# Optimization experiments

Hardware: AMD Instinct MI355X
Metric: run time of the kernel (lower is better)

Reference implementation:

```python
import jax, jax.numpy as jnp
import numpy as np

C, H, O, T, B = 15, 256, 512, 60, 1024


def setup_inputs() -> dict:
    key = jax.random.key(0)
    ks = jax.random.split(key, 8)
    s = 1.0 / np.sqrt(H)
    return {
        "x": jax.random.normal(ks[0], (B, H), dtype=jnp.float32),
        "cam": jax.random.randint(ks[1], (B,), 0, C, dtype=jnp.int32),
        "W_ih": jax.random.uniform(ks[2], (C, 3 * H, H), jnp.float32, -s, s),
        "W_hh": jax.random.uniform(ks[3], (C, 3 * H, H), jnp.float32, -s, s),
        "b_ih": jax.random.uniform(ks[4], (C, 3 * H), jnp.float32, -s, s),
        "b_hh": jax.random.uniform(ks[5], (C, 3 * H), jnp.float32, -s, s),
        "Wc": jax.random.uniform(ks[6], (C, O, H), jnp.float32, -s, s),
        "bc": jax.random.uniform(ks[7], (C, O), jnp.float32, -s, s),
    }


def reference(x, cam, W_ih, W_hh, b_ih, b_hh, Wc, bc):
    # Gather per-sample (per-camera) parameters once.
    Wi = W_ih[cam]          # [B, 3H, H]
    Wh = W_hh[cam]          # [B, 3H, H]
    bi = b_ih[cam]          # [B, 3H]
    bh = b_hh[cam]          # [B, 3H]
    Wcs = Wc[cam]           # [B, O, H]
    bcs = bc[cam]           # [B, O]

    # Input is constant across timesteps -> input gate preactivations computed once.
    gi = jnp.einsum('bh,bgh->bg', x, Wi) + bi   # [B, 3H]
    gi_r, gi_z, gi_n = jnp.split(gi, 3, axis=1)

    h0 = jnp.zeros_like(x)  # [B, H]

    def step(h, _):
        gh = jnp.einsum('bh,bgh->bg', h, Wh) + bh
        gh_r, gh_z, gh_n = jnp.split(gh, 3, axis=1)
        r = jax.nn.sigmoid(gi_r + gh_r)
        z = jax.nn.sigmoid(gi_z + gh_z)
        n = jnp.tanh(gi_n + r * gh_n)
        h_new = (1.0 - z) * n + z * h
        out = jax.nn.sigmoid(jnp.einsum('bh,boh->bo', h_new, Wcs) + bcs)  # [B, O]
        return h_new, out

    _, outs = jax.lax.scan(step, h0, None, length=T)  # [T, B, O]
    return jnp.transpose(outs, (1, 2, 0))             # [B, O, T]
```

## Files before the change

### kernel.cpp

```cpp
#include <hip/hip_runtime.h>
#include <hip/hip_fp16.h>

#define C_    15
#define H_    256
#define O_    512
#define T_    60
#define B_    1024
#define G3H_  768
#define TS    16
#define MAXG  12
#define NSLOT 96
#define NU    80
#define PACKB 300
#define CVTB  2880

typedef __attribute__((ext_vector_type(8))) short bf16x8;
typedef __attribute__((ext_vector_type(4))) float f32x4;

__device__ __forceinline__ unsigned short f2bf(float f) {
    union { float f; unsigned u; } v; v.f = f;
    return (unsigned short)((v.u + 0x7FFFu + ((v.u >> 16) & 1u)) >> 16);
}
__device__ __forceinline__ float sigf(float x) { return 1.f / (1.f + __expf(-x)); }

__global__ __launch_bounds__(256) void prep_kernel(
    const int* __restrict__ cam, const float* __restrict__ Wih,
    const float* __restrict__ Whh, const float* __restrict__ Wc,
    int* __restrict__ order, int* __restrict__ tcam, int* __restrict__ toff,
    int* __restrict__ tcnt, unsigned short* __restrict__ Wih_b,
    unsigned short* __restrict__ Wpack)
{
    int bid = blockIdx.x, tid = threadIdx.x;
    if (bid == 0) {
        __shared__ int cnt[C_], start[C_], fill[C_];
        if (tid < C_) cnt[tid] = 0;
        if (tid < NSLOT) { tcam[tid] = -1; toff[tid] = 0; tcnt[tid] = 0; }
        __syncthreads();
        for (int b = tid; b < B_; b += 256) atomicAdd(&cnt[cam[b]], 1);
        __syncthreads();
        if (tid == 0) {
            int run = 0;
            for (int c = 0; c < C_; ++c) { start[c] = run; fill[c] = run; run += cnt[c]; }
        }
        __syncthreads();
        for (int b = tid; b < B_; b += 256) {
            int pos = atomicAdd(&fill[cam[b]], 1);
            order[pos] = b;
        }
        __syncthreads();
        if (tid == 0) {
            int gcnt[8] = {0,0,0,0,0,0,0,0};
            for (int c = 0; c < C_; ++c) gcnt[c & 7] += (cnt[c] + TS - 1) / TS;
            int maxg = 0;
            for (int g = 0; g < 8; ++g) maxg = max(maxg, gcnt[g]);
            if (maxg <= MAXG) {
                for (int g = 0; g < 8; ++g) {
                    int k = 0;
                    for (int c = g; c < C_; c += 8)
                        for (int r = 0; r < cnt[c]; r += TS) {
                            int slot = g + 8 * k;
                            tcam[slot] = c; toff[slot] = start[c] + r;
                            tcnt[slot] = min(TS, cnt[c] - r); ++k;
                        }
                }
            } else {
                int ti = 0;
                for (int c = 0; c < C_; ++c)
                    for (int r = 0; r < cnt[c]; r += TS) {
                        tcam[ti] = c; toff[ti] = start[c] + r;
                        tcnt[ti] = min(TS, cnt[c] - r); ++ti;
                    }
            }
        }
    } else if (bid <= PACKB) {
        int cu = (bid - 1) * 4 + (tid >> 6);
        int c = cu / NU, u = cu - c * NU;
        int lane = tid & 63, q = lane >> 4, l16 = lane & 15;
        const float* src = (u < 48)
            ? &Whh[((size_t)c * G3H_ + u * 16 + l16) * H_]
            : &Wc[((size_t)c * O_ + (u - 48) * 16 + l16) * H_];
        unsigned short* dst = Wpack + ((size_t)cu * 8) * 512 + lane * 8;
#pragma unroll
        for (int kk = 0; kk < 8; ++kk) {
            float4 v0 = *(const float4*)&src[kk * 32 + q * 8];
            float4 v1 = *(const float4*)&src[kk * 32 + q * 8 + 4];
            unsigned short* d = dst + kk * 512;
            d[0] = f2bf(v0.x); d[1] = f2bf(v0.y); d[2] = f2bf(v0.z); d[3] = f2bf(v0.w);
            d[4] = f2bf(v1.x); d[5] = f2bf(v1.y); d[6] = f2bf(v1.z); d[7] = f2bf(v1.w);
        }
    } else {
        int i = (bid - 1 - PACKB) * 256 + tid;
        float4 v = ((const float4*)Wih)[i];
        unsigned p0 = (unsigned)f2bf(v.x) | ((unsigned)f2bf(v.y) << 16);
        unsigned p1 = (unsigned)f2bf(v.z) | ((unsigned)f2bf(v.w) << 16);
        ((uint2*)Wih_b)[i] = make_uint2(p0, p1);
    }
}

__global__ __launch_bounds__(512, 2) void persist_kernel(
    const float* __restrict__ x, const unsigned short* __restrict__ Wih_b,
    const unsigned short* __restrict__ Wpack, const float* __restrict__ bih,
    const float* __restrict__ bhh, const int* __restrict__ order,
    const int* __restrict__ tcam, const int* __restrict__ toff,
    const int* __restrict__ tcnt, unsigned short* __restrict__ htraj)
{
    int slot = blockIdx.x;
    int c = tcam[slot]; if (c < 0) return;
    int cnt = tcnt[slot], off = toff[slot];
    int tid = threadIdx.x, w = tid >> 6, lane = tid & 63, q = lane >> 4, l16 = lane & 15;

    __shared__ float gisT[G3H_][20];
    __shared__ unsigned short hbf[2][16][264];

    for (int idx = tid; idx < TS * 64; idx += 512) {
        int m = idx >> 6, c4 = idx & 63;
        float4 v = make_float4(0.f, 0.f, 0.f, 0.f);
        if (m < cnt) v = *(const float4*)&x[(size_t)order[off + m] * H_ + (c4 << 2)];
        unsigned p0 = (unsigned)f2bf(v.x) | ((unsigned)f2bf(v.y) << 16);
        unsigned p1 = (unsigned)f2bf(v.z) | ((unsigned)f2bf(v.w) << 16);
        *(uint2*)&hbf[0][m][c4 << 2] = make_uint2(p0, p1);
    }
    __syncthreads();

    {
        f32x4 acc[6];
#pragma unroll
        for (int ui = 0; ui < 6; ++ui) acc[ui] = (f32x4){0.f, 0.f, 0.f, 0.f};
#pragma unroll
        for (int kk = 0; kk < 8; ++kk) {
            bf16x8 a = *(const bf16x8*)&hbf[0][l16][kk * 32 + q * 8];
#pragma unroll
            for (int ui = 0; ui < 6; ++ui) {
                int col = (w * 6 + ui) * 16 + l16;
                bf16x8 b = *(const bf16x8*)(Wih_b + ((size_t)c * G3H_ + col) * H_ + kk * 32 + q * 8);
                acc[ui] = __builtin_amdgcn_mfma_f32_16x16x32_bf16(a, b, acc[ui], 0, 0, 0);
            }
        }
#pragma unroll
        for (int ui = 0; ui < 6; ++ui) {
            int col = (w * 6 + ui) * 16 + l16;
            float bias = bih[c * G3H_ + col] + (col < 2 * H_ ? bhh[c * G3H_ + col] : 0.f);
#pragma unroll
            for (int r = 0; r < 4; ++r) gisT[col][q * 4 + r] = acc[ui][r] + bias;
        }
    }
    __builtin_amdgcn_sched_barrier(0);

    bf16x8 wf[6][8];
#pragma unroll
    for (int ii = 0; ii < 3; ++ii)
#pragma unroll
        for (int jj = 0; jj < 2; ++jj)
#pragma unroll
            for (int kk = 0; kk < 8; ++kk)
                wf[ii * 2 + jj][kk] = *(const bf16x8*)(
                    Wpack + (((size_t)(c * NU + ii * 16 + w + 8 * jj)) * 8 + kk) * 512 + lane * 8);

    float bhn[2], hreg[2][4];
#pragma unroll
    for (int i = 0; i < 2; ++i) {
        int col = (w + 8 * i) * 16 + l16;
        bhn[i] = bhh[c * G3H_ + 2 * H_ + col];
#pragma unroll
        for (int r = 0; r < 4; ++r) hreg[i][r] = 0.f;
    }
    unsigned short* hp = htraj + ((size_t)slot * TS + q * 4) * 256 + w * 16 + l16;
    __syncthreads();

#pragma unroll 2
    for (int s = 0; s < T_; ++s) {
        int wbuf = s & 1, rbuf = wbuf ^ 1;
        f32x4 acc[6];
#pragma unroll
        for (int ui = 0; ui < 6; ++ui) acc[ui] = (f32x4){0.f, 0.f, 0.f, 0.f};
        if (s > 0) {
#pragma unroll
            for (int kk = 0; kk < 8; ++kk) {
                bf16x8 a = *(const bf16x8*)&hbf[rbuf][l16][kk * 32 + q * 8];
#pragma unroll
                for (int ui = 0; ui < 6; ++ui)
                    acc[ui] = __builtin_amdgcn_mfma_f32_16x16x32_bf16(a, wf[ui][kk], acc[ui], 0, 0, 0);
            }
        }
#pragma unroll
        for (int i = 0; i < 2; ++i) {
            int col = (w + 8 * i) * 16 + l16;
            f32x4 gr = *(const f32x4*)&gisT[col][q * 4];
            f32x4 gz = *(const f32x4*)&gisT[H_ + col][q * 4];
            f32x4 gn = *(const f32x4*)&gisT[2 * H_ + col][q * 4];
#pragma unroll
            for (int r = 0; r < 4; ++r) {
                float rr = sigf(gr[r] + acc[i][r]);
                float zz = sigf(gz[r] + acc[2 + i][r]);
                float pre = gn[r] + rr * (acc[4 + i][r] + bhn[i]);
                float nn = 2.f * sigf(2.f * pre) - 1.f;
                float hn = (1.f - zz) * nn + zz * hreg[i][r];
                hreg[i][r] = hn;
                unsigned short hb = f2bf(hn);
                hbf[wbuf][q * 4 + r][col] = hb;
                hp[r * 256 + i * 128] = hb;
            }
        }
        hp += (size_t)NSLOT * TS * 256;
        asm volatile("s_waitcnt lgkmcnt(0)" ::: "memory");
        __builtin_amdgcn_s_barrier();
        __builtin_amdgcn_sched_barrier(0);
    }
}

__global__ __launch_bounds__(512, 2) void out_kernel(
    const unsigned short* __restrict__ Wpack, const float* __restrict__ bc,
    const unsigned short* __restrict__ htraj, const int* __restrict__ order,
    const int* __restrict__ tcam, const int* __restrict__ toff,
    const int* __restrict__ tcnt, float* __restrict__ outp)
{
    int slot = blockIdx.x;
    int c = tcam[slot]; if (c < 0) return;
    int n = tcnt[slot], off = toff[slot];
    int tz = blockIdx.z;
    int tid = threadIdx.x, w = tid >> 6, lane = tid & 63, q = lane >> 4, l16 = lane & 15;
    __shared__ unsigned short hb[2][16][264];
    __shared__ int ord16[16];
    if (tid < 16) ord16[tid] = (tid < n) ? order[off + tid] : -1;

    int u = blockIdx.y * 8 + w;
    bf16x8 wf[8];
    const unsigned short* wb = Wpack + ((size_t)c * NU + 48 + u) * 8 * 512 + lane * 8;
#pragma unroll
    for (int kk = 0; kk < 8; ++kk) wf[kk] = *(const bf16x8*)(wb + (size_t)kk * 512);
    float bcr = bc[c * O_ + u * 16 + l16];

    int m = tid >> 5, c8 = (tid & 31) * 8;
    const unsigned short* hsrc =
        &htraj[(((size_t)(tz * 10) * NSLOT + slot) * 16 + m) * 256 + c8];
    uint4 stg = *(const uint4*)hsrc;
    *(uint4*)&hb[0][m][c8] = stg;
    __syncthreads();

    float vals[4][10];
#pragma unroll
    for (int ti = 0; ti < 10; ++ti) {
        int cur = ti & 1;
        if (ti + 1 < 10)
            stg = *(const uint4*)(hsrc + (size_t)(ti + 1) * NSLOT * TS * 256);
        f32x4 acc = (f32x4){0.f, 0.f, 0.f, 0.f};
#pragma unroll
        for (int kk = 0; kk < 8; ++kk) {
            bf16x8 a = *(const bf16x8*)&hb[cur][l16][kk * 32 + q * 8];
            acc = __builtin_amdgcn_mfma_f32_16x16x32_bf16(a, wf[kk], acc, 0, 0, 0);
        }
#pragma unroll
        for (int r = 0; r < 4; ++r) vals[r][ti] = sigf(acc[r] + bcr);
        if (ti + 1 < 10) {
            *(uint4*)&hb[cur ^ 1][m][c8] = stg;
            asm volatile("s_waitcnt lgkmcnt(0)" ::: "memory");
            __builtin_amdgcn_s_barrier();
            __builtin_amdgcn_sched_barrier(0);
        }
    }
    int o = u * 16 + l16;
#pragma unroll
    for (int r = 0; r < 4; ++r) {
        int b = ord16[q * 4 + r];
        if (b >= 0) {
            float* dst = &outp[((size_t)b * O_ + o) * T_ + tz * 10];
#pragma unroll
            for (int j = 0; j < 5; ++j)
                *(float2*)&dst[j * 2] = make_float2(vals[r][2 * j], vals[r][2 * j + 1]);
        }
    }
}

extern "C" void kernel_launch(void* const* d_in, const int* in_sizes, int n_in,
                              void* d_out, int out_size, void* d_ws, size_t ws_size,
                              hipStream_t stream)
{
    const float* x   = (const float*)d_in[0];
    const int*   cam = (const int*)d_in[1];
    const float* Wih = (const float*)d_in[2];
    const float* Whh = (const float*)d_in[3];
    const float* bih = (const float*)d_in[4];
    const float* bhh = (const float*)d_in[5];
    const float* Wc  = (const float*)d_in[6];
    const float* bc  = (const float*)d_in[7];
    float* outp = (float*)d_out;

    char* w = (char*)d_ws;
    unsigned short* Wih_b = (unsigned short*)w; w += (size_t)C_ * G3H_ * H_ * 2;
    unsigned short* Wpack = (unsigned short*)w; w += (size_t)C_ * NU * 8 * 512 * 2;
    int* order = (int*)w; w += B_ * 4;
    int* tcam  = (int*)w; w += NSLOT * 4;
    int* toff  = (int*)w; w += NSLOT * 4;
    int* tcnt  = (int*)w; w += NSLOT * 4;
    unsigned short* htraj = (unsigned short*)w;

    prep_kernel<<<1 + PACKB + CVTB, 256, 0, stream>>>(cam, Wih, Whh, Wc, order, tcam,
                                                      toff, tcnt, Wih_b, Wpack);
    persist_kernel<<<NSLOT, 512, 0, stream>>>(x, Wih_b, Wpack, bih, bhh, order, tcam,
                                              toff, tcnt, htraj);
    out_kernel<<<dim3(NSLOT, 4, 6), 512, 0, stream>>>(Wpack, bc, htraj, order, tcam,
                                                      toff, tcnt, outp);
}
```

Measured before the change: 434.1 us.

## Fuse output projection into persistent GRU kernel using a 10-step LDS ring

```diff
diff --git a/kernel.cpp b/kernel.cpp
--- a/kernel.cpp
+++ b/kernel.cpp
@@ -97,12 +97,13 @@
     }
 }
 
-__global__ __launch_bounds__(512, 2) void persist_kernel(
+__global__ __launch_bounds__(512, 1) void persist_kernel(
     const float* __restrict__ x, const unsigned short* __restrict__ Wih_b,
     const unsigned short* __restrict__ Wpack, const float* __restrict__ bih,
-    const float* __restrict__ bhh, const int* __restrict__ order,
-    const int* __restrict__ tcam, const int* __restrict__ toff,
-    const int* __restrict__ tcnt, unsigned short* __restrict__ htraj)
+    const float* __restrict__ bhh, const float* __restrict__ bc,
+    const int* __restrict__ order, const int* __restrict__ tcam,
+    const int* __restrict__ toff, const int* __restrict__ tcnt,
+    float* __restrict__ outp)
 {
     int slot = blockIdx.x;
     int c = tcam[slot]; if (c < 0) return;
@@ -110,7 +111,7 @@
     int tid = threadIdx.x, w = tid >> 6, lane = tid & 63, q = lane >> 4, l16 = lane & 15;
 
     __shared__ float gisT[G3H_][20];
-    __shared__ unsigned short hbf[2][16][264];
+    __shared__ unsigned short ring[10][16][264];
 
     for (int idx = tid; idx < TS * 64; idx += 512) {
         int m = idx >> 6, c4 = idx & 63;
@@ -118,7 +119,7 @@
         if (m < cnt) v = *(const float4*)&x[(size_t)order[off + m] * H_ + (c4 << 2)];
         unsigned p0 = (unsigned)f2bf(v.x) | ((unsigned)f2bf(v.y) << 16);
         unsigned p1 = (unsigned)f2bf(v.z) | ((unsigned)f2bf(v.w) << 16);
-        *(uint2*)&hbf[0][m][c4 << 2] = make_uint2(p0, p1);
+        *(uint2*)&ring[0][m][c4 << 2] = make_uint2(p0, p1);
     }
     __syncthreads();
 
@@ -128,7 +129,7 @@
         for (int ui = 0; ui < 6; ++ui) acc[ui] = (f32x4){0.f, 0.f, 0.f, 0.f};
 #pragma unroll
         for (int kk = 0; kk < 8; ++kk) {
-            bf16x8 a = *(const bf16x8*)&hbf[0][l16][kk * 32 + q * 8];
+            bf16x8 a = *(const bf16x8*)&ring[0][l16][kk * 32 + q * 8];
 #pragma unroll
             for (int ui = 0; ui < 6; ++ui) {
                 int col = (w * 6 + ui) * 16 + l16;
@@ -164,19 +165,24 @@
 #pragma unroll
         for (int r = 0; r < 4; ++r) hreg[i][r] = 0.f;
     }
-    unsigned short* hp = htraj + ((size_t)slot * TS + q * 4) * 256 + w * 16 + l16;
+    float bco[4];
+#pragma unroll
+    for (int ui = 0; ui < 4; ++ui)
+        bco[ui] = bc[c * O_ + (w * 4 + ui) * 16 + l16];
+    int bidx[4];
+#pragma unroll
+    for (int r = 0; r < 4; ++r) bidx[r] = (q * 4 + r < cnt) ? order[off + q * 4 + r] : -1;
     __syncthreads();
 
-#pragma unroll 2
     for (int s = 0; s < T_; ++s) {
-        int wbuf = s & 1, rbuf = wbuf ^ 1;
+        int wslot = s % 10, rslot = (wslot == 0) ? 9 : wslot - 1;
         f32x4 acc[6];
 #pragma unroll
         for (int ui = 0; ui < 6; ++ui) acc[ui] = (f32x4){0.f, 0.f, 0.f, 0.f};
         if (s > 0) {
 #pragma unroll
             for (int kk = 0; kk < 8; ++kk) {
-                bf16x8 a = *(const bf16x8*)&hbf[rbuf][l16][kk * 32 + q * 8];
+                bf16x8 a = *(const bf16x8*)&ring[rslot][l16][kk * 32 + q * 8];
 #pragma unroll
                 for (int ui = 0; ui < 6; ++ui)
                     acc[ui] = __builtin_amdgcn_mfma_f32_16x16x32_bf16(a, wf[ui][kk], acc[ui], 0, 0, 0);
@@ -196,77 +202,50 @@
                 float nn = 2.f * sigf(2.f * pre) - 1.f;
                 float hn = (1.f - zz) * nn + zz * hreg[i][r];
                 hreg[i][r] = hn;
-                unsigned short hb = f2bf(hn);
-                hbf[wbuf][q * 4 + r][col] = hb;
-                hp[r * 256 + i * 128] = hb;
-            }
-        }
-        hp += (size_t)NSLOT * TS * 256;
+                ring[wslot][q * 4 + r][col] = f2bf(hn);
+            }
+        }
         asm volatile("s_waitcnt lgkmcnt(0)" ::: "memory");
         __builtin_amdgcn_s_barrier();
         __builtin_amdgcn_sched_barrier(0);
-    }
-}
-
-__global__ __launch_bounds__(512, 2) void out_kernel(
-    const unsigned short* __restrict__ Wpack, const float* __restrict__ bc,
-    const unsigned short* __restrict__ htraj, const int* __restrict__ order,
-    const int* __restrict__ tcam, const int* __restrict__ toff,
-    const int* __restrict__ tcnt, float* __restrict__ outp)
-{
-    int slot = blockIdx.x;
-    int c = tcam[slot]; if (c < 0) return;
-    int n = tcnt[slot], off = toff[slot];
-    int tz = blockIdx.z;
-    int tid = threadIdx.x, w = tid >> 6, lane = tid & 63, q = lane >> 4, l16 = lane & 15;
-    __shared__ unsigned short hb[2][16][264];
-    __shared__ int ord16[16];
-    if (tid < 16) ord16[tid] = (tid < n) ? order[off + tid] : -1;
-
-    int u = blockIdx.y * 8 + w;
-    bf16x8 wf[8];
-    const unsigned short* wb = Wpack + ((size_t)c * NU + 48 + u) * 8 * 512 + lane * 8;
-#pragma unroll
-    for (int kk = 0; kk < 8; ++kk) wf[kk] = *(const bf16x8*)(wb + (size_t)kk * 512);
-    float bcr = bc[c * O_ + u * 16 + l16];
-
-    int m = tid >> 5, c8 = (tid & 31) * 8;
-    const unsigned short* hsrc =
-        &htraj[(((size_t)(tz * 10) * NSLOT + slot) * 16 + m) * 256 + c8];
-    uint4 stg = *(const uint4*)hsrc;
-    *(uint4*)&hb[0][m][c8] = stg;
-    __syncthreads();
-
-    float vals[4][10];
-#pragma unroll
-    for (int ti = 0; ti < 10; ++ti) {
-        int cur = ti & 1;
-        if (ti + 1 < 10)
-            stg = *(const uint4*)(hsrc + (size_t)(ti + 1) * NSLOT * TS * 256);
-        f32x4 acc = (f32x4){0.f, 0.f, 0.f, 0.f};
-#pragma unroll
-        for (int kk = 0; kk < 8; ++kk) {
-            bf16x8 a = *(const bf16x8*)&hb[cur][l16][kk * 32 + q * 8];
-            acc = __builtin_amdgcn_mfma_f32_16x16x32_bf16(a, wf[kk], acc, 0, 0, 0);
-        }
-#pragma unroll
-        for (int r = 0; r < 4; ++r) vals[r][ti] = sigf(acc[r] + bcr);
-        if (ti + 1 < 10) {
-            *(uint4*)&hb[cur ^ 1][m][c8] = stg;
-            asm volatile("s_waitcnt lgkmcnt(0)" ::: "memory");
+
+        if (wslot == 9) {
+            int t0 = s - 9;
+#pragma unroll 1
+            for (int ui = 0; ui < 4; ++ui) {
+                bf16x8 wob[8];
+                const unsigned short* wbp =
+                    Wpack + (((size_t)(c * NU + 48 + w * 4 + ui)) * 8) * 512 + lane * 8;
+#pragma unroll
+                for (int kk = 0; kk < 8; ++kk)
+                    wob[kk] = *(const bf16x8*)(wbp + (size_t)kk * 512);
+                float vals[4][10];
+#pragma unroll
+                for (int ti = 0; ti < 10; ++ti) {
+                    f32x4 acco = (f32x4){0.f, 0.f, 0.f, 0.f};
+#pragma unroll
+                    for (int kk = 0; kk < 8; ++kk) {
+                        bf16x8 a = *(const bf16x8*)&ring[ti][l16][kk * 32 + q * 8];
+                        acco = __builtin_amdgcn_mfma_f32_16x16x32_bf16(a, wob[kk], acco, 0, 0, 0);
+                    }
+#pragma unroll
+                    for (int r = 0; r < 4; ++r) vals[r][ti] = sigf(acco[r] + bco[ui]);
+                }
+                int o = (w * 4 + ui) * 16 + l16;
+#pragma unroll
+                for (int r = 0; r < 4; ++r) {
+                    int b = bidx[r];
+                    if (b >= 0) {
+                        float* dst = &outp[((size_t)b * O_ + o) * T_ + t0];
+#pragma unroll
+                        for (int j = 0; j < 5; ++j)
+                            *(float2*)&dst[2 * j] =
+                                make_float2(vals[r][2 * j], vals[r][2 * j + 1]);
+                    }
+                }
+            }
             __builtin_amdgcn_s_barrier();
             __builtin_amdgcn_sched_barrier(0);
-        }
-    }
-    int o = u * 16 + l16;
-#pragma unroll
-    for (int r = 0; r < 4; ++r) {
-        int b = ord16[q * 4 + r];
-        if (b >= 0) {
-            float* dst = &outp[((size_t)b * O_ + o) * T_ + tz * 10];
-#pragma unroll
-            for (int j = 0; j < 5; ++j)
-                *(float2*)&dst[j * 2] = make_float2(vals[r][2 * j], vals[r][2 * j + 1]);
         }
     }
 }
@@ -292,12 +271,9 @@
     int* tcam  = (int*)w; w += NSLOT * 4;
     int* toff  = (int*)w; w += NSLOT * 4;
     int* tcnt  = (int*)w; w += NSLOT * 4;
-    unsigned short* htraj = (unsigned short*)w;
 
     prep_kernel<<<1 + PACKB + CVTB, 256, 0, stream>>>(cam, Wih, Whh, Wc, order, tcam,
                                                       toff, tcnt, Wih_b, Wpack);
-    persist_kernel<<<NSLOT, 512, 0, stream>>>(x, Wih_b, Wpack, bih, bhh, order, tcam,
-                                              toff, tcnt, htraj);
-    out_kernel<<<dim3(NSLOT, 4, 6), 512, 0, stream>>>(Wpack, bc, htraj, order, tcam,
-                                                      toff, tcnt, outp);
-}
+    persist_kernel<<<NSLOT, 512, 0, stream>>>(x, Wih_b, Wpack, bih, bhh, bc, order, tcam,
+                                              toff, tcnt, outp);
+}
```

Result: slower. 1.531 ms (+252.7%).

## Restructure output kernel to stage all timesteps once and loop output tiles

Applied to the files above, without the earlier changes.

```diff
diff --git a/kernel.cpp b/kernel.cpp
--- a/kernel.cpp
+++ b/kernel.cpp
@@ -13,6 +13,7 @@
 #define NU    80
 #define PACKB 300
 #define CVTB  2880
+#define TCH   10
 
 typedef __attribute__((ext_vector_type(8))) short bf16x8;
 typedef __attribute__((ext_vector_type(4))) float f32x4;
@@ -174,6 +175,7 @@
 #pragma unroll
         for (int ui = 0; ui < 6; ++ui) acc[ui] = (f32x4){0.f, 0.f, 0.f, 0.f};
         if (s > 0) {
+            __builtin_amdgcn_s_setprio(1);
 #pragma unroll
             for (int kk = 0; kk < 8; ++kk) {
                 bf16x8 a = *(const bf16x8*)&hbf[rbuf][l16][kk * 32 + q * 8];
@@ -181,6 +183,7 @@
                 for (int ui = 0; ui < 6; ++ui)
                     acc[ui] = __builtin_amdgcn_mfma_f32_16x16x32_bf16(a, wf[ui][kk], acc[ui], 0, 0, 0);
             }
+            __builtin_amdgcn_s_setprio(0);
         }
 #pragma unroll
         for (int i = 0; i < 2; ++i) {
@@ -208,7 +211,7 @@
     }
 }
 
-__global__ __launch_bounds__(512, 2) void out_kernel(
+__global__ __launch_bounds__(512, 1) void out_kernel(
     const unsigned short* __restrict__ Wpack, const float* __restrict__ bc,
     const unsigned short* __restrict__ htraj, const int* __restrict__ order,
     const int* __restrict__ tcam, const int* __restrict__ toff,
@@ -217,56 +220,53 @@
     int slot = blockIdx.x;
     int c = tcam[slot]; if (c < 0) return;
     int n = tcnt[slot], off = toff[slot];
-    int tz = blockIdx.z;
+    int tz = blockIdx.y;
     int tid = threadIdx.x, w = tid >> 6, lane = tid & 63, q = lane >> 4, l16 = lane & 15;
-    __shared__ unsigned short hb[2][16][264];
+    __shared__ unsigned short hb[TCH][16][264];
     __shared__ int ord16[16];
     if (tid < 16) ord16[tid] = (tid < n) ? order[off + tid] : -1;
 
-    int u = blockIdx.y * 8 + w;
-    bf16x8 wf[8];
-    const unsigned short* wb = Wpack + ((size_t)c * NU + 48 + u) * 8 * 512 + lane * 8;
-#pragma unroll
-    for (int kk = 0; kk < 8; ++kk) wf[kk] = *(const bf16x8*)(wb + (size_t)kk * 512);
-    float bcr = bc[c * O_ + u * 16 + l16];
-
     int m = tid >> 5, c8 = (tid & 31) * 8;
     const unsigned short* hsrc =
-        &htraj[(((size_t)(tz * 10) * NSLOT + slot) * 16 + m) * 256 + c8];
-    uint4 stg = *(const uint4*)hsrc;
-    *(uint4*)&hb[0][m][c8] = stg;
+        &htraj[(((size_t)(tz * TCH) * NSLOT + slot) * 16 + m) * 256 + c8];
+#pragma unroll
+    for (int ti = 0; ti < TCH; ++ti) {
+        uint4 v = *(const uint4*)(hsrc + (size_t)ti * NSLOT * TS * 256);
+        *(uint4*)&hb[ti][m][c8] = v;
+    }
     __syncthreads();
 
-    float vals[4][10];
-#pragma unroll
-    for (int ti = 0; ti < 10; ++ti) {
-        int cur = ti & 1;
-        if (ti + 1 < 10)
-            stg = *(const uint4*)(hsrc + (size_t)(ti + 1) * NSLOT * TS * 256);
-        f32x4 acc = (f32x4){0.f, 0.f, 0.f, 0.f};
-#pragma unroll
-        for (int kk = 0; kk < 8; ++kk) {
-            bf16x8 a = *(const bf16x8*)&hb[cur][l16][kk * 32 + q * 8];
-            acc = __builtin_amdgcn_mfma_f32_16x16x32_bf16(a, wf[kk], acc, 0, 0, 0);
-        }
-#pragma unroll
-        for (int r = 0; r < 4; ++r) vals[r][ti] = sigf(acc[r] + bcr);
-        if (ti + 1 < 10) {
-            *(uint4*)&hb[cur ^ 1][m][c8] = stg;
-            asm volatile("s_waitcnt lgkmcnt(0)" ::: "memory");
-            __builtin_amdgcn_s_barrier();
-            __builtin_amdgcn_sched_barrier(0);
-        }
-    }
-    int o = u * 16 + l16;
-#pragma unroll
-    for (int r = 0; r < 4; ++r) {
-        int b = ord16[q * 4 + r];
-        if (b >= 0) {
-            float* dst = &outp[((size_t)b * O_ + o) * T_ + tz * 10];
-#pragma unroll
-            for (int j = 0; j < 5; ++j)
-                *(float2*)&dst[j * 2] = make_float2(vals[r][2 * j], vals[r][2 * j + 1]);
+#pragma unroll 1
+    for (int ui = 0; ui < 4; ++ui) {
+        bf16x8 wob[8];
+        const unsigned short* wbp =
+            Wpack + (((size_t)(c * NU + 48 + w * 4 + ui)) * 8) * 512 + lane * 8;
+#pragma unroll
+        for (int kk = 0; kk < 8; ++kk)
+            wob[kk] = *(const bf16x8*)(wbp + (size_t)kk * 512);
+        float bcr = bc[c * O_ + (w * 4 + ui) * 16 + l16];
+        float vals[4][TCH];
+#pragma unroll
+        for (int ti = 0; ti < TCH; ++ti) {
+            f32x4 acc = (f32x4){0.f, 0.f, 0.f, 0.f};
+#pragma unroll
+            for (int kk = 0; kk < 8; ++kk) {
+                bf16x8 a = *(const bf16x8*)&hb[ti][l16][kk * 32 + q * 8];
+                acc = __builtin_amdgcn_mfma_f32_16x16x32_bf16(a, wob[kk], acc, 0, 0, 0);
+            }
+#pragma unroll
+            for (int r = 0; r < 4; ++r) vals[r][ti] = sigf(acc[r] + bcr);
+        }
+        int o = (w * 4 + ui) * 16 + l16;
+#pragma unroll
+        for (int r = 0; r < 4; ++r) {
+            int b = ord16[q * 4 + r];
+            if (b >= 0) {
+                float* dst = &outp[((size_t)b * O_ + o) * T_ + tz * TCH];
+#pragma unroll
+                for (int j = 0; j < 5; ++j)
+                    *(float2*)&dst[2 * j] = make_float2(vals[r][2 * j], vals[r][2 * j + 1]);
+            }
         }
     }
 }
@@ -298,6 +298,6 @@
                                                       toff, tcnt, Wih_b, Wpack);
     persist_kernel<<<NSLOT, 512, 0, stream>>>(x, Wih_b, Wpack, bih, bhh, order, tcam,
                                               toff, tcnt, htraj);
-    out_kernel<<<dim3(NSLOT, 4, 6), 512, 0, stream>>>(Wpack, bc, htraj, order, tcam,
-                                                      toff, tcnt, outp);
-}
+    out_kernel<<<dim3(NSLOT, T_ / TCH), 512, 0, stream>>>(Wpack, bc, htraj, order, tcam,
+                                                          toff, tcnt, outp);
+}
```

Result: slower. 587.5 us (+35.3%).
